# Performance work log

Measured on AMD Instinct MI355X. Metric: run time of the kernel, lower is better.

Reference implementation:

```python
import jax, jax.numpy as jnp
import numpy as np

C, H, W, B = 64, 64, 64, 8

def setup_inputs() -> dict:
    key = jax.random.key(0)
    ks = jax.random.split(key, 6)
    s = 0.05
    return {
        "x": jax.random.normal(ks[0], (B, C, H, W), dtype=jnp.float32),
        "w_cam": jax.random.normal(ks[1], (C, C), dtype=jnp.float32) * s,        # CAM 1x1 conv
        "w_q": jax.random.normal(ks[2], (C // 2, C), dtype=jnp.float32) * s,     # SAM query 1x1 conv
        "w_k": jax.random.normal(ks[3], (C // 2, C), dtype=jnp.float32) * s,     # SAM key 1x1 conv
        "w_v": jax.random.normal(ks[4], (C, C), dtype=jnp.float32) * s,          # SAM value 1x1 conv
        "w_bn": jax.random.normal(ks[5], (C, 2 * C), dtype=jnp.float32) * s,     # bottleneck 1x1 conv 2c->c
    }

def _conv1x1(w, x):
    # w: [O, C], x: [B, C, H, W] -> [B, O, H, W]
    return jnp.einsum('oc,bchw->bohw', w, x)

def reference(x, w_cam, w_q, w_k, w_v, w_bn):
    b, c, h, w = x.shape
    hw = h * w
    # ---- CAM (channel attention) ----
    xc = _conv1x1(w_cam, x).reshape(b, c, hw)            # [b, c, hw]
    energy_c = jnp.einsum('bcn,bdn->bcd', xc, xc)        # [b, c, c]
    attn_c = jax.nn.softmax(energy_c, axis=-1)           # dropout = identity (eval)
    out_c = jnp.einsum('bcd,bdn->bcn', attn_c, x.reshape(b, c, hw)).reshape(b, c, h, w)
    # ---- SAM (spatial attention) ----
    q = _conv1x1(w_q, x).reshape(b, c // 2, hw)          # [b, c/2, hw]
    k = _conv1x1(w_k, x).reshape(b, c // 2, hw)
    v = _conv1x1(w_v, x).reshape(b, c, hw)
    energy_s = jnp.einsum('bcn,bcm->bnm', q, k)          # [b, hw, hw]
    attn_s = jax.nn.softmax(energy_s, axis=-1)           # dropout = identity (eval)
    out_s = jnp.einsum('bcm,bnm->bcn', v, attn_s).reshape(b, c, h, w)
    # ---- fuse: concat -> bottleneck 1x1 conv -> residual ----
    cat = jnp.concatenate([out_c, out_s], axis=1)        # [b, 2c, h, w]
    out = _conv1x1(w_bn, cat)                            # [b, c, h, w]
    return x + out
```

## Files before the change

### kernel.cpp

```cpp
#include <hip/hip_runtime.h>

#define BB 8
#define C 64
#define HW 4096

typedef __attribute__((ext_vector_type(8))) __bf16 bf16x8;
typedef __attribute__((ext_vector_type(16))) float f32x16;
typedef unsigned int uint;
typedef unsigned short ushort;

__device__ __forceinline__ ushort bfb(float f) {
  return __builtin_bit_cast(ushort, (__bf16)f);
}
__device__ __forceinline__ uint pk2(float a, float b) {
  return (uint)bfb(a) | ((uint)bfb(b) << 16);
}
__device__ __forceinline__ uint cvtpk(float a, float b) {
  uint r;
  asm("v_cvt_pk_bf16_f32 %0, %1, %2" : "=v"(r) : "v"(a), "v"(b));
  return r;
}
__device__ __forceinline__ f32x16 mfma_bf16(bf16x8 a, bf16x8 b, f32x16 c) {
  return __builtin_amdgcn_mfma_f32_32x32x16_bf16(a, b, c, 0, 0, 0);
}

__global__ __launch_bounds__(128) void gram_fold_kernel(const float* __restrict__ x,
                                                        float* __restrict__ G,
                                                        const float* __restrict__ w_bn,
                                                        const float* __restrict__ w_q,
                                                        const float* __restrict__ w_k,
                                                        const float* __restrict__ w_v,
                                                        char* __restrict__ wall) {
  const int bxx = blockIdx.x;
  const int t = threadIdx.x;
  if (bxx < 8) {
    const int slot = bxx * 2 + (t >> 6);
    const int ot = slot >> 2, kc = slot & 3;
    const int l = t & 63, lo5 = l & 31, hi = l >> 5;
    float v[8];
    if (ot == 0) {
#pragma unroll
      for (int j = 0; j < 8; ++j)
        v[j] = 1.44269504088896f * w_q[lo5 * 64 + kc * 16 + hi * 8 + j];
    } else if (ot == 1) {
#pragma unroll
      for (int j = 0; j < 8; ++j) v[j] = w_k[lo5 * 64 + kc * 16 + hi * 8 + j];
    } else {
      int c = (ot - 2) * 32 + lo5;
#pragma unroll
      for (int j = 0; j < 8; ++j) {
        int d = kc * 16 + hi * 8 + j;
        float acc = 0.f;
        for (int e = 0; e < 64; ++e) acc += w_bn[c * 128 + 64 + e] * w_v[e * 64 + d];
        v[j] = acc;
      }
    }
    uint4 w;
    w.x = pk2(v[0], v[1]); w.y = pk2(v[2], v[3]);
    w.z = pk2(v[4], v[5]); w.w = pk2(v[6], v[7]);
    *(uint4*)(wall + slot * 1024 + l * 16) = w;
    return;
  }
  const int bx = bxx - 8;
  const int b = bx >> 5, ch = bx & 31;
  const int wv = t >> 6, l = t & 63, lo5 = l & 31, hi = l >> 5;
  const int n0 = ch * 128 + wv * 64;
  const float* xb = x + (size_t)b * C * HW;
  f32x16 fz;
#pragma unroll
  for (int r = 0; r < 16; ++r) fz[r] = 0.f;
  f32x16 a00 = fz, a01 = fz, a10 = fz, a11 = fz;
#pragma unroll 1
  for (int kc = 0; kc < 4; ++kc) {
    int nb = n0 + kc * 16 + hi * 8;
    const float4* p0 = (const float4*)(xb + (size_t)lo5 * HW + nb);
    const float4* p1 = (const float4*)(xb + (size_t)(32 + lo5) * HW + nb);
    float v0[8], v1[8];
    {
      float4 a = p0[0], bq = p0[1];
      v0[0] = a.x; v0[1] = a.y; v0[2] = a.z; v0[3] = a.w;
      v0[4] = bq.x; v0[5] = bq.y; v0[6] = bq.z; v0[7] = bq.w;
      float4 c = p1[0], d = p1[1];
      v1[0] = c.x; v1[1] = c.y; v1[2] = c.z; v1[3] = c.w;
      v1[4] = d.x; v1[5] = d.y; v1[6] = d.z; v1[7] = d.w;
    }
    uint4 uh0, ul0, uh1, ul1;
    {
      float h[8], e[8];
#pragma unroll
      for (int j = 0; j < 8; ++j) { h[j] = (float)(__bf16)v0[j]; e[j] = v0[j] - h[j]; }
      uh0.x = pk2(h[0], h[1]); uh0.y = pk2(h[2], h[3]); uh0.z = pk2(h[4], h[5]); uh0.w = pk2(h[6], h[7]);
      ul0.x = cvtpk(e[0], e[1]); ul0.y = cvtpk(e[2], e[3]); ul0.z = cvtpk(e[4], e[5]); ul0.w = cvtpk(e[6], e[7]);
#pragma unroll
      for (int j = 0; j < 8; ++j) { h[j] = (float)(__bf16)v1[j]; e[j] = v1[j] - h[j]; }
      uh1.x = pk2(h[0], h[1]); uh1.y = pk2(h[2], h[3]); uh1.z = pk2(h[4], h[5]); uh1.w = pk2(h[6], h[7]);
      ul1.x = cvtpk(e[0], e[1]); ul1.y = cvtpk(e[2], e[3]); ul1.z = cvtpk(e[4], e[5]); ul1.w = cvtpk(e[6], e[7]);
    }
    bf16x8 f0h = __builtin_bit_cast(bf16x8, uh0);
    bf16x8 f0l = __builtin_bit_cast(bf16x8, ul0);
    bf16x8 f1h = __builtin_bit_cast(bf16x8, uh1);
    bf16x8 f1l = __builtin_bit_cast(bf16x8, ul1);
    a00 = mfma_bf16(f0h, f0h, a00); a00 = mfma_bf16(f0h, f0l, a00); a00 = mfma_bf16(f0l, f0h, a00);
    a01 = mfma_bf16(f0h, f1h, a01); a01 = mfma_bf16(f0h, f1l, a01); a01 = mfma_bf16(f0l, f1h, a01);
    a10 = mfma_bf16(f1h, f0h, a10); a10 = mfma_bf16(f1h, f0l, a10); a10 = mfma_bf16(f1l, f0h, a10);
    a11 = mfma_bf16(f1h, f1h, a11); a11 = mfma_bf16(f1h, f1l, a11); a11 = mfma_bf16(f1l, f1h, a11);
  }
  float* g = G + (size_t)b * 4096;
#pragma unroll
  for (int r = 0; r < 16; ++r) {
    int row = (r & 3) + 8 * (r >> 2) + 4 * hi;
    atomicAdd(&g[row * 64 + lo5], a00[r]);
    atomicAdd(&g[row * 64 + 32 + lo5], a01[r]);
    atomicAdd(&g[(32 + row) * 64 + lo5], a10[r]);
    atomicAdd(&g[(32 + row) * 64 + 32 + lo5], a11[r]);
  }
}

__device__ __forceinline__ void cam_body(const float* __restrict__ G,
                                         const float* __restrict__ w_cam,
                                         const float* __restrict__ w_bn,
                                         float* __restrict__ m1,
                                         int b, float* buf) {
  const int t = threadIdx.x;
#pragma unroll
  for (int i = 0; i < 16; ++i) {
    int idx = t + i * 256;
    buf[idx] = G[(size_t)b * 4096 + idx];
  }
  __syncthreads();
  const int lane = t & 63, rg = (t >> 6) * 16;
  float acc[16];
#pragma unroll
  for (int r = 0; r < 16; ++r) acc[r] = 0.f;
  for (int c = 0; c < 64; ++c) {
    float g = buf[c * 64 + lane];
#pragma unroll
    for (int r = 0; r < 16; ++r) acc[r] += w_cam[(rg + r) * 64 + c] * g;
  }
  __syncthreads();
#pragma unroll
  for (int r = 0; r < 16; ++r) buf[(rg + r) * 64 + lane] = acc[r];
  __syncthreads();
#pragma unroll
  for (int r = 0; r < 16; ++r) acc[r] = 0.f;
  for (int d = 0; d < 64; ++d) {
    float wl = w_cam[lane * 64 + d];
#pragma unroll
    for (int r = 0; r < 16; ++r) acc[r] += buf[(rg + r) * 64 + d] * wl;
  }
  __syncthreads();
#pragma unroll
  for (int r = 0; r < 16; ++r) buf[(rg + r) * 64 + lane] = acc[r];
  __syncthreads();
  {
    int row = t >> 2, c0 = (t & 3) * 16;
    float v[16];
    float mx = -1e30f;
#pragma unroll
    for (int j = 0; j < 16; ++j) { v[j] = buf[row * 64 + c0 + j]; mx = fmaxf(mx, v[j]); }
    mx = fmaxf(mx, __shfl_xor(mx, 1));
    mx = fmaxf(mx, __shfl_xor(mx, 2));
    float s = 0.f;
#pragma unroll
    for (int j = 0; j < 16; ++j) { v[j] = __expf(v[j] - mx); s += v[j]; }
    s += __shfl_xor(s, 1);
    s += __shfl_xor(s, 2);
    float inv = 1.f / s;
#pragma unroll
    for (int j = 0; j < 16; ++j) buf[row * 64 + c0 + j] = v[j] * inv;
  }
  __syncthreads();
  float a2[16];
#pragma unroll
  for (int dd = 0; dd < 16; ++dd) a2[dd] = 0.f;
  for (int r = 0; r < 64; ++r) {
    float wv = w_bn[lane * 128 + r];
#pragma unroll
    for (int dd = 0; dd < 16; ++dd) a2[dd] += wv * buf[r * 64 + rg + dd];
  }
  float* mb = m1 + (size_t)b * 4096;
#pragma unroll
  for (int dd = 0; dd < 16; ++dd) mb[(rg + dd) * 64 + lane] = a2[dd];
}

__global__ __launch_bounds__(256) void prep_cam_kernel(const float* __restrict__ x,
                                                       const char* __restrict__ wall,
                                                       char* __restrict__ qd2,
                                                       char* __restrict__ kd2,
                                                       char* __restrict__ vpd2,
                                                       const float* __restrict__ G,
                                                       const float* __restrict__ w_cam,
                                                       const float* __restrict__ w_bn,
                                                       float* __restrict__ m1) {
  __shared__ float buf[4096];
  const int bxx = blockIdx.x;
  if (bxx < 8) {
    cam_body(G, w_cam, w_bn, m1, bxx, buf);
    return;
  }
  const int bx = bxx - 8;
  const int b = bx >> 5, nt2 = bx & 31;
  const int t = threadIdx.x;
  const int wv = t >> 6, l = t & 63, lo5 = l & 31, hi = l >> 5;
  const int chunk = nt2 * 4 + wv;
  const int n0 = chunk * 32;
  const int tt = chunk >> 1;
  const int n = n0 + lo5;
  const float* xb = x + (size_t)b * C * HW;

  f32x16 fz;
#pragma unroll
  for (int r = 0; r < 16; ++r) fz[r] = 0.f;

  bf16x8 xf[4];
#pragma unroll
  for (int kc = 0; kc < 4; ++kc) {
    float xv[8];
#pragma unroll
    for (int j = 0; j < 8; ++j)
      xv[j] = xb[(size_t)(kc * 16 + hi * 8 + j) * HW + n];
    uint4 u;
    u.x = cvtpk(xv[0], xv[1]); u.y = cvtpk(xv[2], xv[3]);
    u.z = cvtpk(xv[4], xv[5]); u.w = cvtpk(xv[6], xv[7]);
    xf[kc] = __builtin_bit_cast(bf16x8, u);
  }

#pragma unroll
  for (int ot = 0; ot < 4; ++ot) {
    f32x16 acc = fz;
#pragma unroll
    for (int kc = 0; kc < 4; ++kc) {
      bf16x8 wf = *(const bf16x8*)(wall + ((ot << 2) | kc) * 1024 + l * 16);
      acc = (ot < 2) ? mfma_bf16(wf, xf[kc], acc)
                     : mfma_bf16(xf[kc], wf, acc);
    }
    uint wlo[8], whi[8];
#pragma unroll
    for (int i2 = 0; i2 < 8; ++i2) {
      uint w = cvtpk(acc[2 * i2], acc[2 * i2 + 1]);
      uint p = __shfl_xor(w, 32);
      wlo[i2] = hi ? p : w;
      whi[i2] = hi ? w : p;
    }
    uint4 u40, u41;
    u40.x = hi ? wlo[4] : wlo[0];
    u40.y = hi ? wlo[5] : wlo[1];
    u40.z = hi ? whi[4] : whi[0];
    u40.w = hi ? whi[5] : whi[1];
    u41.x = hi ? wlo[6] : wlo[2];
    u41.y = hi ? wlo[7] : wlo[3];
    u41.z = hi ? whi[6] : whi[2];
    u41.w = hi ? whi[7] : whi[3];
    const int e0 = hi * 2;
    if (ot == 0) {
      char* p = qd2 + ((size_t)b * HW + n) * 64;
      *(uint4*)(p + e0 * 16) = u40;
      *(uint4*)(p + (e0 + 1) * 16) = u41;
    } else if (ot == 1) {
      char* p = kd2 + ((size_t)(b * 64 + tt)) * 4096 + (chunk & 1) * 2048 + (n & 31) * 16;
      *(uint4*)(p + e0 * 512) = u40;
      *(uint4*)(p + (e0 + 1) * 512) = u41;
    } else {
      int c = ((ot - 2) << 5) + lo5;
      int oct0 = (chunk & 1) * 4;
      char* p = vpd2 + ((size_t)(b * 64 + tt)) * 8192 + (c >> 5) * 4096 + (c & 31) * 16;
      *(uint4*)(p + (oct0 + e0) * 512) = u40;
      *(uint4*)(p + (oct0 + e0 + 1) * 512) = u41;
    }
  }
}

__global__ __launch_bounds__(256) void fa_kernel(const char* __restrict__ qd2,
                                                 const char* __restrict__ kd2,
                                                 const char* __restrict__ vpd2,
                                                 char* __restrict__ op,
                                                 float* __restrict__ lp) {
  const int t = threadIdx.x;
  const int l = t & 63, lo5 = l & 31, hi = l >> 5;
  const int wv = t >> 6;
  const int bx = blockIdx.x;
  const int g = (bx & 7) | ((bx >> 8) << 3);
  const int qt = (bx >> 3) & 31;
  const int b = g >> 2, kvs = g & 3;
  const int nq = qt * 128 + wv * 32 + lo5;

  const char* qb = qd2 + ((size_t)b * HW + nq) * 64;
  bf16x8 qf0 = *(const bf16x8*)(qb + hi * 16);
  bf16x8 qf1 = *(const bf16x8*)(qb + 32 + hi * 16);

  f32x16 fz;
#pragma unroll
  for (int r = 0; r < 16; ++r) fz[r] = 0.f;
  f32x16 o0 = fz, o1 = fz;
  float lrun = 0.f;

  const char* kbase = kd2 + ((size_t)(b * 64 + kvs * 16)) * 4096 + l * 16;
  const char* vbase = vpd2 + ((size_t)(b * 64 + kvs * 16)) * 8192 + l * 16;

  bf16x8 kf0 = *(const bf16x8*)(kbase);
  bf16x8 kf1 = *(const bf16x8*)(kbase + 1024);
  bf16x8 kf2 = *(const bf16x8*)(kbase + 2048);
  bf16x8 kf3 = *(const bf16x8*)(kbase + 3072);

#pragma unroll 1
  for (int i = 0; i < 16; ++i) {
    bf16x8 kn0, kn1, kn2, kn3;
    if (i < 15) {
      const char* kn = kbase + (size_t)(i + 1) * 4096;
      kn0 = *(const bf16x8*)(kn);
      kn1 = *(const bf16x8*)(kn + 1024);
      kn2 = *(const bf16x8*)(kn + 2048);
      kn3 = *(const bf16x8*)(kn + 3072);
    }
    const char* vb = vbase + (size_t)i * 8192;
    bf16x8 vfa[4], vfb[4];
#pragma unroll
    for (int ks = 0; ks < 4; ++ks) {
      vfa[ks] = *(const bf16x8*)(vb + ks * 1024);
      vfb[ks] = *(const bf16x8*)(vb + 4096 + ks * 1024);
    }
    f32x16 s0 = mfma_bf16(kf0, qf0, fz);
    s0 = mfma_bf16(kf1, qf1, s0);
    f32x16 s1 = mfma_bf16(kf2, qf0, fz);
    s1 = mfma_bf16(kf3, qf1, s1);
    float ps = 0.f;
#pragma unroll
    for (int r = 0; r < 16; ++r) {
      s0[r] = __builtin_amdgcn_exp2f(s0[r]);
      ps += s0[r];
    }
#pragma unroll
    for (int r = 0; r < 16; ++r) {
      s1[r] = __builtin_amdgcn_exp2f(s1[r]);
      ps += s1[r];
    }
    lrun += ps;
#pragma unroll
    for (int ks = 0; ks < 4; ++ks) {
      const f32x16& pm = (ks < 2) ? s0 : s1;
      const int rb = (ks & 1) * 8;
      uint w0 = cvtpk(pm[rb + 0], pm[rb + 1]);
      uint w1 = cvtpk(pm[rb + 2], pm[rb + 3]);
      uint w2 = cvtpk(pm[rb + 4], pm[rb + 5]);
      uint w3 = cvtpk(pm[rb + 6], pm[rb + 7]);
      uint x0 = __shfl_xor(w0, 32);
      uint x1 = __shfl_xor(w1, 32);
      uint x2 = __shfl_xor(w2, 32);
      uint x3 = __shfl_xor(w3, 32);
      uint4 fw;
      fw.x = hi ? x2 : w0;
      fw.y = hi ? x3 : w1;
      fw.z = hi ? w2 : x0;
      fw.w = hi ? w3 : x1;
      bf16x8 pf = __builtin_bit_cast(bf16x8, fw);
      o0 = mfma_bf16(vfa[ks], pf, o0);
      o1 = mfma_bf16(vfb[ks], pf, o1);
    }
    kf0 = kn0; kf1 = kn1; kf2 = kn2; kf3 = kn3;
  }
  lrun += __shfl_xor(lrun, 32);

  ushort* opu = (ushort*)op;
  const size_t obase = ((size_t)(b * 64) * 4 + kvs) * HW + nq;
#pragma unroll
  for (int r = 0; r < 16; ++r) {
    int c0 = (r & 3) + 8 * (r >> 2) + 4 * hi;
    opu[obase + (size_t)c0 * 4 * HW] = bfb(o0[r]);
    opu[obase + (size_t)(c0 + 32) * 4 * HW] = bfb(o1[r]);
  }
  if (hi == 0) lp[(size_t)(kvs * 8 + b) * HW + nq] = lrun;
}

__global__ __launch_bounds__(256) void final_kernel(const float* __restrict__ x,
                                                    const float* __restrict__ m1,
                                                    const char* __restrict__ op,
                                                    const float* __restrict__ lp,
                                                    float* __restrict__ outp) {
  __shared__ __align__(16) float xt[4096];
  __shared__ __align__(16) float ms[4096];
  const int b = blockIdx.y, tt = blockIdx.x, t = threadIdx.x;
  const float4* xg = (const float4*)(x + (size_t)b * C * HW);
  float4* xt4 = (float4*)xt;
#pragma unroll
  for (int i = 0; i < 4; ++i) {
    int idx = t + i * 256;
    int c = idx >> 4, ng = idx & 15;
    xt4[c * 16 + (ng ^ (c & 15))] = xg[c * 1024 + tt * 16 + ng];
  }
  float4* ms4 = (float4*)ms;
  const float4* mg = (const float4*)(m1 + (size_t)b * 4096);
#pragma unroll
  for (int i = 0; i < 4; ++i) ms4[t + i * 256] = mg[t + i * 256];
  __syncthreads();
  const int n = t & 63, sub = t >> 6;
  const int gn = tt * 64 + n;
  float xr[64];
#pragma unroll
  for (int c = 0; c < 64; ++c)
    xr[c] = xt[c * 64 + (((n >> 2) ^ (c & 15)) << 2) + (n & 3)];
  float lsum = 0.f;
#pragma unroll
  for (int kvs = 0; kvs < 4; ++kvs) lsum += lp[(size_t)(kvs * 8 + b) * HW + gn];
  float linv = 1.f / lsum;
  const ushort* opu = (const ushort*)op;
  float acc[16];
#pragma unroll
  for (int ci = 0; ci < 16; ++ci) {
    int c = sub * 16 + ci;
    float osum = 0.f;
#pragma unroll
    for (int kvs = 0; kvs < 4; ++kvs) {
      ushort u = opu[((size_t)(b * 64 + c) * 4 + kvs) * HW + gn];
      osum += __builtin_bit_cast(float, (uint)u << 16);
    }
    acc[ci] = xr[c] + osum * linv;
  }
  for (int d = 0; d < 64; ++d) {
    float xv = xr[d];
    const float4* mr = (const float4*)(ms + d * 64 + sub * 16);
#pragma unroll
    for (int c4 = 0; c4 < 4; ++c4) {
      float4 mv = mr[c4];
      acc[c4 * 4 + 0] += mv.x * xv;
      acc[c4 * 4 + 1] += mv.y * xv;
      acc[c4 * 4 + 2] += mv.z * xv;
      acc[c4 * 4 + 3] += mv.w * xv;
    }
  }
  float* ob = outp + (size_t)b * C * HW + gn;
#pragma unroll
  for (int ci = 0; ci < 16; ++ci)
    ob[(size_t)(sub * 16 + ci) * HW] = acc[ci];
}

extern "C" void kernel_launch(void* const* d_in, const int* in_sizes, int n_in,
                              void* d_out, int out_size, void* d_ws, size_t ws_size,
                              hipStream_t stream) {
  const float* x     = (const float*)d_in[0];
  const float* w_cam = (const float*)d_in[1];
  const float* w_q   = (const float*)d_in[2];
  const float* w_k   = (const float*)d_in[3];
  const float* w_v   = (const float*)d_in[4];
  const float* w_bn  = (const float*)d_in[5];
  float* out = (float*)d_out;
  char* wsb = (char*)d_ws;

  char*  wall = wsb;
  float* m1   = (float*)(wsb + 16384);
  float* G    = (float*)(wsb + 147456);
  char*  qd2  = wsb + 278528;
  char*  kd2  = qd2 + 2097152;
  char*  vpd2 = kd2 + 2097152;
  float* lp   = (float*)(vpd2 + 4194304);
  char*  op   = (char*)lp + 524288;

  hipMemsetAsync(G, 0, (size_t)BB * 4096 * sizeof(float), stream);
  gram_fold_kernel<<<264, 128, 0, stream>>>(x, G, w_bn, w_q, w_k, w_v, wall);
  prep_cam_kernel<<<264, 256, 0, stream>>>(x, wall, qd2, kd2, vpd2, G, w_cam, w_bn, m1);
  fa_kernel<<<1024, 256, 0, stream>>>(qd2, kd2, vpd2, op, lp);
  final_kernel<<<dim3(64, BB), 256, 0, stream>>>(x, m1, op, lp, out);
}
```

Before: 126.9 us.

## Reduce Gram matrix per batch in shared memory instead of global atomics

The Gram kernel becomes 9 blocks of 1024 threads, one block per batch plus one for the weight fold. Each of the 16 waves accumulates a quarter-K slice, and the partials are summed in shared memory before a plain store. This removes the memset and the global atomicAdds. The cost is a much smaller grid: 8 blocks now read all of x, which leaves most CUs idle and may make this stage memory-latency bound.

After: 135.6 us. +6.9%, slower.

```diff
diff --git a/kernel.cpp b/kernel.cpp
--- a/kernel.cpp
+++ b/kernel.cpp
@@ -24,17 +24,18 @@
   return __builtin_amdgcn_mfma_f32_32x32x16_bf16(a, b, c, 0, 0, 0);
 }
 
-__global__ __launch_bounds__(128) void gram_fold_kernel(const float* __restrict__ x,
-                                                        float* __restrict__ G,
-                                                        const float* __restrict__ w_bn,
-                                                        const float* __restrict__ w_q,
-                                                        const float* __restrict__ w_k,
-                                                        const float* __restrict__ w_v,
-                                                        char* __restrict__ wall) {
+__global__ __launch_bounds__(1024) void gram_fold_kernel(const float* __restrict__ x,
+                                                         float* __restrict__ G,
+                                                         const float* __restrict__ w_bn,
+                                                         const float* __restrict__ w_q,
+                                                         const float* __restrict__ w_k,
+                                                         const float* __restrict__ w_v,
+                                                         char* __restrict__ wall) {
+  __shared__ float slots[4][4096];
   const int bxx = blockIdx.x;
   const int t = threadIdx.x;
-  if (bxx < 8) {
-    const int slot = bxx * 2 + (t >> 6);
+  if (bxx == 0) {
+    const int slot = t >> 6;
     const int ot = slot >> 2, kc = slot & 3;
     const int l = t & 63, lo5 = l & 31, hi = l >> 5;
     float v[8];
@@ -61,18 +62,17 @@
     *(uint4*)(wall + slot * 1024 + l * 16) = w;
     return;
   }
-  const int bx = bxx - 8;
-  const int b = bx >> 5, ch = bx & 31;
-  const int wv = t >> 6, l = t & 63, lo5 = l & 31, hi = l >> 5;
-  const int n0 = ch * 128 + wv * 64;
+  const int b = bxx - 1;
+  const int w = t >> 6, l = t & 63, lo5 = l & 31, hi = l >> 5;
   const float* xb = x + (size_t)b * C * HW;
   f32x16 fz;
 #pragma unroll
   for (int r = 0; r < 16; ++r) fz[r] = 0.f;
   f32x16 a00 = fz, a01 = fz, a10 = fz, a11 = fz;
+  const int k0 = w * 256;
 #pragma unroll 1
-  for (int kc = 0; kc < 4; ++kc) {
-    int nb = n0 + kc * 16 + hi * 8;
+  for (int kc = 0; kc < 16; ++kc) {
+    int nb = k0 + kc * 16 + hi * 8;
     const float4* p0 = (const float4*)(xb + (size_t)lo5 * HW + nb);
     const float4* p1 = (const float4*)(xb + (size_t)(32 + lo5) * HW + nb);
     float v0[8], v1[8];
@@ -105,14 +105,37 @@
     a10 = mfma_bf16(f1h, f0h, a10); a10 = mfma_bf16(f1h, f0l, a10); a10 = mfma_bf16(f1l, f0h, a10);
     a11 = mfma_bf16(f1h, f1h, a11); a11 = mfma_bf16(f1h, f1l, a11); a11 = mfma_bf16(f1l, f1h, a11);
   }
+  const int sl = w & 3, rnd = w >> 2;
+  if (rnd == 0) {
+#pragma unroll
+    for (int r = 0; r < 16; ++r) {
+      int row = (r & 3) + 8 * (r >> 2) + 4 * hi;
+      slots[sl][row * 64 + lo5] = a00[r];
+      slots[sl][row * 64 + 32 + lo5] = a01[r];
+      slots[sl][(32 + row) * 64 + lo5] = a10[r];
+      slots[sl][(32 + row) * 64 + 32 + lo5] = a11[r];
+    }
+  }
+  __syncthreads();
+#pragma unroll 1
+  for (int R = 1; R < 4; ++R) {
+    if (rnd == R) {
+#pragma unroll
+      for (int r = 0; r < 16; ++r) {
+        int row = (r & 3) + 8 * (r >> 2) + 4 * hi;
+        slots[sl][row * 64 + lo5] += a00[r];
+        slots[sl][row * 64 + 32 + lo5] += a01[r];
+        slots[sl][(32 + row) * 64 + lo5] += a10[r];
+        slots[sl][(32 + row) * 64 + 32 + lo5] += a11[r];
+      }
+    }
+    __syncthreads();
+  }
   float* g = G + (size_t)b * 4096;
 #pragma unroll
-  for (int r = 0; r < 16; ++r) {
-    int row = (r & 3) + 8 * (r >> 2) + 4 * hi;
-    atomicAdd(&g[row * 64 + lo5], a00[r]);
-    atomicAdd(&g[row * 64 + 32 + lo5], a01[r]);
-    atomicAdd(&g[(32 + row) * 64 + lo5], a10[r]);
-    atomicAdd(&g[(32 + row) * 64 + 32 + lo5], a11[r]);
+  for (int i = 0; i < 4; ++i) {
+    int idx = t + i * 1024;
+    g[idx] = slots[0][idx] + slots[1][idx] + slots[2][idx] + slots[3][idx];
   }
 }
 
@@ -454,8 +477,7 @@
   float* lp   = (float*)(vpd2 + 4194304);
   char*  op   = (char*)lp + 524288;
 
-  hipMemsetAsync(G, 0, (size_t)BB * 4096 * sizeof(float), stream);
-  gram_fold_kernel<<<264, 128, 0, stream>>>(x, G, w_bn, w_q, w_k, w_v, wall);
+  gram_fold_kernel<<<9, 1024, 0, stream>>>(x, G, w_bn, w_q, w_k, w_v, wall);
   prep_cam_kernel<<<264, 256, 0, stream>>>(x, wall, qd2, kd2, vpd2, G, w_cam, w_bn, m1);
   fa_kernel<<<1024, 256, 0, stream>>>(qd2, kd2, vpd2, op, lp);
   final_kernel<<<dim3(64, BB), 256, 0, stream>>>(x, m1, op, lp, out);
```
